# Performance work log

Measured on AMD Instinct MI355X. Metric: run time of the kernel, lower is better.

## Reference

```python
import jax, jax.numpy as jnp
import numpy as np

N = 200000      # total nodes
E = 800000      # directed edges
G = 4096        # graphs in batch
D_DRUG = 128
D_CELL = 954
HID = 128
OUT = 128
EPS = 1e-5      # BatchNorm eps


def _bn(x, gamma, beta):
    # training-mode BatchNorm1d (batch statistics, biased var), dropout is eval/identity
    m = jnp.mean(x, axis=0)
    v = jnp.mean((x - m) ** 2, axis=0)
    return gamma * (x - m) * jax.lax.rsqrt(v + EPS) + beta


def _gcn_conv(x, edge_index, W, b):
    # PyG GCNConv: add self-loops, symmetric normalization, aggregate, then bias
    src = jnp.concatenate([edge_index[0], jnp.arange(N)])
    dst = jnp.concatenate([edge_index[1], jnp.arange(N)])
    ones = jnp.ones(src.shape[0], dtype=x.dtype)
    deg = jax.ops.segment_sum(ones, dst, num_segments=N)
    dinv = jnp.where(deg > 0, jax.lax.rsqrt(jnp.maximum(deg, 1.0)), 0.0)
    norm = dinv[src] * dinv[dst]                      # [E+N]
    h = x @ W                                         # [N, out]
    msg = h[src] * norm[:, None]                      # gather + scale
    out = jax.ops.segment_sum(msg, dst, num_segments=N)  # scatter-add
    return out + b


def setup_inputs() -> dict:
    key = jax.random.key(0)
    ks = jax.random.split(key, 12)
    x = jax.random.normal(ks[0], (N, D_DRUG), jnp.float32)
    edge_index = jax.random.randint(ks[1], (2, E), 0, N)
    ibatch = (jnp.arange(N) * G) // N  # sorted, every graph non-empty
    gexpr = jax.random.normal(ks[2], (G, D_CELL), jnp.float32)

    def w(k, shape):
        return jax.random.normal(k, shape, jnp.float32) / np.float32(np.sqrt(shape[0]))

    return {
        "x": x, "edge_index": edge_index, "ibatch": ibatch, "gexpr": gexpr,
        "W1": w(ks[3], (D_DRUG, HID)), "b1": jnp.zeros((HID,), jnp.float32),
        "g1": jnp.ones((HID,), jnp.float32), "be1": jnp.zeros((HID,), jnp.float32),
        "W2": w(ks[4], (HID, OUT)), "b2": jnp.zeros((OUT,), jnp.float32),
        "g2": jnp.ones((OUT,), jnp.float32), "be2": jnp.zeros((OUT,), jnp.float32),
        "Wc1": w(ks[5], (D_CELL, HID)), "bc1": jnp.zeros((HID,), jnp.float32),
        "gc": jnp.ones((HID,), jnp.float32), "bec": jnp.zeros((HID,), jnp.float32),
        "Wc2": w(ks[6], (HID, OUT)), "bc2": jnp.zeros((OUT,), jnp.float32),
    }


def reference(x, edge_index, ibatch, gexpr,
              W1, b1, g1, be1, W2, b2, g2, be2,
              Wc1, bc1, gc, bec, Wc2, bc2):
    # drug branch
    h = _gcn_conv(x, edge_index, W1, b1)
    h = _bn(jax.nn.relu(h), g1, be1)
    h = _gcn_conv(h, edge_index, W2, b2)
    h = _bn(jax.nn.relu(h), g2, be2)
    x_drug = jax.ops.segment_max(h, ibatch, num_segments=G)  # global_max_pool
    # cellline branch
    c = jnp.tanh(gexpr @ Wc1 + bc1)
    c = _bn(c, gc, bec)
    x_cell = jax.nn.relu(c @ Wc2 + bc2)
    return x_drug, x_cell
```

## Files before the change

kernel.cpp:

```cpp
#include <hip/hip_runtime.h>

#define NFEAT 128

typedef __attribute__((ext_vector_type(4))) float f32x4;
typedef __attribute__((ext_vector_type(8))) short bf16x8;

__device__ __forceinline__ unsigned short f2bf(float f) {
    unsigned u = __builtin_bit_cast(unsigned, f);
    u += 0x7fffu + ((u >> 16) & 1u);
    return (unsigned short)(u >> 16);
}
__device__ __forceinline__ float bf2f(unsigned short s) {
    unsigned u = ((unsigned)s) << 16;
    return __builtin_bit_cast(float, u);
}

__device__ __forceinline__ void dma16(const void* g, void* l) {
    __builtin_amdgcn_global_load_lds(
        (const __attribute__((address_space(1))) unsigned int*)g,
        (__attribute__((address_space(3))) unsigned int*)l, 16, 0, 0);
}

template <int ACT, typename OutT, typename AT>
__device__ __forceinline__ void gemm_loop(
    int tfirst, int tstride, int tcount, int by,
    const AT* __restrict__ A, const unsigned short* __restrict__ Bt,
    OutT* __restrict__ C, int M, int ldA, int ldB,
    const float* __restrict__ bias, const float* __restrict__ dscale, char* smem)
{
    constexpr bool AF32 = (sizeof(AT) == 4);
    AT* buf0 = (AT*)smem;
    AT* buf1 = buf0 + 64 * 128;
    const int tid = threadIdx.x;
    const int wv = tid >> 6, lane = tid & 63;
    const int l16 = lane & 15, quad = lane >> 4;
    const int kbase = by * 128;

    const int nc0 = (wv & 1) * 64;
    bf16x8 bfr[4][4];
#pragma unroll
    for (int nt = 0; nt < 4; ++nt) {
        const unsigned short* bp =
            Bt + (size_t)(nc0 + nt * 16 + l16) * ldB + kbase + quad * 8;
#pragma unroll
        for (int ks = 0; ks < 4; ++ks)
            bfr[nt][ks] = *(const bf16x8*)(bp + ks * 32);
    }

    C += (size_t)by * M * NFEAT;
    const int rh = wv >> 1;
    const int r0 = wv * 16;

    auto stage = [&](AT* dst, long tile) {
        const long t0 = tile * 64;
        if constexpr (AF32) {
#pragma unroll
            for (int j = 0; j < 8; ++j) {
                const float* gp = (const float*)A +
                    (size_t)(t0 + r0 + j * 2 + (lane >> 5)) * ldA + kbase +
                    (lane & 31) * 4;
                dma16(gp, (void*)&dst[(r0 + j * 2) * 128]);
            }
        } else {
#pragma unroll
            for (int j = 0; j < 4; ++j) {
                const unsigned short* gp = (const unsigned short*)A +
                    (size_t)(t0 + r0 + j * 4 + (lane >> 4)) * ldA + kbase +
                    l16 * 8;
                dma16(gp, (void*)&dst[(r0 + j * 4) * 128]);
            }
        }
    };

    if (tfirst < tcount) stage(buf0, tfirst);
    __syncthreads();

    int cur = 0;
    for (long t = tfirst; t < tcount; t += tstride) {
        AT* bufc = cur ? buf1 : buf0;
        AT* bufn = cur ? buf0 : buf1;
        const long tn = t + tstride;
        if (tn < tcount) stage(bufn, tn);

        bf16x8 af[2][4];
#pragma unroll
        for (int mt = 0; mt < 2; ++mt) {
            const int row = rh * 32 + mt * 16 + l16;
#pragma unroll
            for (int ks = 0; ks < 4; ++ks) {
                if constexpr (AF32) {
                    const float* lp = (const float*)bufc + row * 128 + ks * 32 + quad * 8;
                    f32x4 v0 = *(const f32x4*)lp;
                    f32x4 v1 = *(const f32x4*)(lp + 4);
                    bf16x8 tt;
                    tt[0] = (short)f2bf(v0[0]); tt[1] = (short)f2bf(v0[1]);
                    tt[2] = (short)f2bf(v0[2]); tt[3] = (short)f2bf(v0[3]);
                    tt[4] = (short)f2bf(v1[0]); tt[5] = (short)f2bf(v1[1]);
                    tt[6] = (short)f2bf(v1[2]); tt[7] = (short)f2bf(v1[3]);
                    af[mt][ks] = tt;
                } else {
                    af[mt][ks] = *(const bf16x8*)((const unsigned short*)bufc +
                                                  row * 128 + ks * 32 + quad * 8);
                }
            }
        }

        f32x4 acc[2][4];
#pragma unroll
        for (int a = 0; a < 2; ++a)
#pragma unroll
            for (int b = 0; b < 4; ++b) acc[a][b] = (f32x4){0.f, 0.f, 0.f, 0.f};
#pragma unroll
        for (int ks = 0; ks < 4; ++ks)
#pragma unroll
            for (int nt = 0; nt < 4; ++nt)
#pragma unroll
                for (int mt = 0; mt < 2; ++mt)
                    acc[mt][nt] = __builtin_amdgcn_mfma_f32_16x16x32_bf16(
                        af[mt][ks], bfr[nt][ks], acc[mt][nt], 0, 0, 0);

        const long tile0 = t * 64;
        float ds[2][4];
#pragma unroll
        for (int mt = 0; mt < 2; ++mt)
#pragma unroll
            for (int r = 0; r < 4; ++r) {
                long row = tile0 + rh * 32 + mt * 16 + quad * 4 + r;
                ds[mt][r] = dscale ? dscale[row] : 1.f;
            }
#pragma unroll
        for (int nt = 0; nt < 4; ++nt) {
            int col = nc0 + nt * 16 + l16;
            float bv = bias ? bias[col] : 0.f;
#pragma unroll
            for (int mt = 0; mt < 2; ++mt) {
                long rbase = tile0 + rh * 32 + mt * 16 + quad * 4;
#pragma unroll
                for (int r = 0; r < 4; ++r) {
                    float v = acc[mt][nt][r] + bv;
                    if (ACT == 1) v = tanhf(v);
                    if (ACT == 2) v = fmaxf(v, 0.f);
                    v *= ds[mt][r];
                    if constexpr (sizeof(OutT) == 2)
                        C[(size_t)(rbase + r) * NFEAT + col] = (OutT)f2bf(v);
                    else
                        C[(size_t)(rbase + r) * NFEAT + col] = (OutT)v;
                }
            }
        }
        __syncthreads();
        cur ^= 1;
    }
}

__global__ void k_prep(const float* __restrict__ W1, unsigned short* __restrict__ W1t,
                       const float* __restrict__ Wc1, unsigned short* __restrict__ Wc1t,
                       const float* __restrict__ gexpr, float* __restrict__ Apad,
                       const int* __restrict__ dst, int* __restrict__ deg,
                       int G, int DC, int DCP, int E, int r1, int r2, int r3)
{
    int b = blockIdx.x, t = threadIdx.x;
    if (b < r1) {
        int idx = b * 256 + t;
        int n = idx >> 7, k = idx & 127;
        W1t[idx] = f2bf(W1[(size_t)k * NFEAT + n]);
    } else if (b < r2) {
        int idx = (b - r1) * 256 + t;
        int n = idx >> 10, k = idx & 1023;
        Wc1t[idx] = (k < DC) ? f2bf(Wc1[(size_t)k * NFEAT + n]) : (unsigned short)0;
    } else if (b < r3) {
        long idx = (long)(b - r2) * 256 + t;
        if (idx < (long)G * DCP) {
            long i = idx / DCP; int k = (int)(idx - i * DCP);
            Apad[idx] = (k < DC) ? gexpr[i * DC + k] : 0.f;
        }
    } else {
        int e = (b - r3) * 256 + t;
        if (e < E) atomicAdd(&deg[dst[e]], 1);
    }
}

__device__ __forceinline__ void bnfold_body(
    int bb, const float* __restrict__ sums8, const float* __restrict__ gamma,
    const float* __restrict__ beta, float invN,
    const float* __restrict__ W, const float* __restrict__ extra,
    unsigned short* __restrict__ Wt, float* __restrict__ brow)
{
    __shared__ float ssc[128], ssh[128];
    int t = threadIdx.x;
    if (t < 128) {
        float s = 0.f, s2 = 0.f;
#pragma unroll
        for (int c = 0; c < 8; ++c) { s += sums8[c * 256 + t]; s2 += sums8[c * 256 + 128 + t]; }
        float mean = s * invN;
        float var = s2 * invN - mean * mean;
        float rstd = rsqrtf(fmaxf(var, 0.f) + 1e-5f);
        float sc = gamma[t] * rstd;
        ssc[t] = sc;
        ssh[t] = beta[t] - mean * sc;
    }
    __syncthreads();
    if (bb < 64) {
        int idx = bb * 256 + t;
        int n = idx >> 7, k = idx & 127;
        Wt[idx] = f2bf(W[(size_t)k * NFEAT + n] * ssc[k]);
    } else if (t < 128) {
        float s = extra ? extra[t] : 0.f;
        for (int k = 0; k < 128; ++k) s += ssh[k] * W[(size_t)k * NFEAT + t];
        brow[t] = s;
    }
}

__global__ void k_bnfold2(
    const float* sA, const float* gA, const float* bA, float invA,
    const float* WA, const float* eA, unsigned short* WtA, float* browA,
    const float* sB, const float* gB, const float* bB, float invB,
    const float* WB, const float* eB, unsigned short* WtB, float* browB)
{
    int b = blockIdx.x;
    if (b < 65) bnfold_body(b, sA, gA, bA, invA, WA, eA, WtA, browA);
    else        bnfold_body(b - 65, sB, gB, bB, invB, WB, eB, WtB, browB);
}

__global__ __launch_bounds__(256) void k_scan1(const int* __restrict__ deg,
        int* __restrict__ rowptr, int* __restrict__ bsum, float* __restrict__ dinv, int N)
{
    __shared__ int sh[256];
    int t = threadIdx.x;
    int base = blockIdx.x * 1024 + t * 4;
    int v[4];
#pragma unroll
    for (int j = 0; j < 4; ++j) {
        v[j] = (base + j < N) ? deg[base + j] : 0;
        if (base + j < N) dinv[base + j] = rsqrtf((float)(v[j] + 1));
    }
    int s = v[0] + v[1] + v[2] + v[3];
    sh[t] = s;
    __syncthreads();
    int incl = s;
    for (int off = 1; off < 256; off <<= 1) {
        int x = (t >= off) ? sh[t - off] : 0;
        __syncthreads();
        incl += x;
        sh[t] = incl;
        __syncthreads();
    }
    int run = incl - s;
#pragma unroll
    for (int j = 0; j < 4; ++j) {
        if (base + j < N) rowptr[base + j] = run;
        run += v[j];
    }
    if (t == 255) bsum[blockIdx.x] = incl;
}

__global__ void k_scan2(int* __restrict__ bsum, int nb)
{
    __shared__ int sh[256];
    int t = threadIdx.x;
    int s = (t < nb) ? bsum[t] : 0;
    sh[t] = s;
    __syncthreads();
    int incl = s;
    for (int off = 1; off < 256; off <<= 1) {
        int x = (t >= off) ? sh[t - off] : 0;
        __syncthreads();
        incl += x;
        sh[t] = incl;
        __syncthreads();
    }
    if (t < nb) bsum[t] = incl - s;
}

__global__ void k_scan3(int* __restrict__ rowptr, int* __restrict__ cursor,
                        const int* __restrict__ bsum, int N, int E)
{
    int i = blockIdx.x * 256 + threadIdx.x;
    if (i < N) {
        int v = rowptr[i] + bsum[i >> 10];
        rowptr[i] = v;
        cursor[i] = v;
    } else if (i == N) {
        rowptr[N] = E;
    }
}

__global__ void k_fill(const int* __restrict__ src, const int* __restrict__ dst,
                       int* __restrict__ cursor, int* __restrict__ csr, int E)
{
    int e = blockIdx.x * 256 + threadIdx.x;
    if (e < E) {
        int pos = atomicAdd(&cursor[dst[e]], 1);
        csr[pos] = src[e];
    }
}

__global__ __launch_bounds__(256) void k_pair1(
    const float* __restrict__ x, const unsigned short* __restrict__ W1t,
    unsigned short* __restrict__ h, int N, const float* __restrict__ dinv,
    const float* __restrict__ Apad, const unsigned short* __restrict__ Wc1t,
    float* __restrict__ pbuf, int G, int nb1, int gtiles)
{
    extern __shared__ char smem[];
    int b = blockIdx.x;
    if (b < nb1) {
        gemm_loop<0, unsigned short, float>(b, nb1, gtiles, 0,
                                            x, W1t, h, N, 128, 128,
                                            nullptr, dinv, smem);
    } else {
        int cb = b - nb1;
        gemm_loop<0, float, float>(cb & 15, 16, 64, cb >> 4,
                                   Apad, Wc1t, pbuf, G, 1024, 1024,
                                   nullptr, nullptr, smem);
    }
}

__device__ __forceinline__ void unpack_add(float* acc, uint4 a)
{
    acc[0] += bf2f((unsigned short)(a.x & 0xffff));
    acc[1] += bf2f((unsigned short)(a.x >> 16));
    acc[2] += bf2f((unsigned short)(a.y & 0xffff));
    acc[3] += bf2f((unsigned short)(a.y >> 16));
    acc[4] += bf2f((unsigned short)(a.z & 0xffff));
    acc[5] += bf2f((unsigned short)(a.z >> 16));
    acc[6] += bf2f((unsigned short)(a.w & 0xffff));
    acc[7] += bf2f((unsigned short)(a.w >> 16));
}

__device__ __forceinline__ void row_gather(const unsigned short* __restrict__ h,
    const int* __restrict__ rowptr, const int* __restrict__ csr,
    long i, int f, float* acc)
{
    int lo = rowptr[i], hi = rowptr[i + 1];
    int e = lo;
    for (; e + 3 < hi; e += 4) {
        int s0 = csr[e], s1 = csr[e + 1], s2 = csr[e + 2], s3 = csr[e + 3];
        uint4 a = *(const uint4*)(h + ((size_t)s0 << 7) + f);
        uint4 b = *(const uint4*)(h + ((size_t)s1 << 7) + f);
        uint4 c = *(const uint4*)(h + ((size_t)s2 << 7) + f);
        uint4 d = *(const uint4*)(h + ((size_t)s3 << 7) + f);
        unpack_add(acc, a); unpack_add(acc, b);
        unpack_add(acc, c); unpack_add(acc, d);
    }
    for (; e < hi; ++e) {
        int s0 = csr[e];
        uint4 a = *(const uint4*)(h + ((size_t)s0 << 7) + f);
        unpack_add(acc, a);
    }
    uint4 hs = *(const uint4*)(h + ((size_t)i << 7) + f);
    unpack_add(acc, hs);
}

__global__ __launch_bounds__(256) void k_pair2(
    const unsigned short* __restrict__ h, const int* __restrict__ rowptr,
    const int* __restrict__ csr, const float* __restrict__ dinv,
    const float* __restrict__ bias, unsigned short* __restrict__ out,
    float* __restrict__ sums8, int N, int na,
    const float* __restrict__ p, const float* __restrict__ biasC,
    unsigned short* __restrict__ cbuf, float* __restrict__ sumsC, int G)
{
    __shared__ float red[4][256];
    const int tid = threadIdx.x;
    if (blockIdx.x >= na) {
        int bb = blockIdx.x - na;
        int j = tid & 127;
        int slot = bb * 2 + (tid >> 7);
        const int nslots = 64;
        const size_t st = (size_t)G * NFEAT;
        float b = biasC[j], s = 0.f, s2 = 0.f;
        for (int i = slot; i < G; i += nslots) {
            size_t o = (size_t)i * NFEAT + j;
            float v = b;
#pragma unroll
            for (int c = 0; c < 8; ++c) v += p[o + c * st];
            v = tanhf(v);
            cbuf[o] = f2bf(v);
            s += v; s2 += v * v;
        }
        atomicAdd(&sumsC[(bb & 7) * 256 + j], s);
        atomicAdd(&sumsC[(bb & 7) * 256 + 128 + j], s2);
        return;
    }
    const int wv = tid >> 6, lane = tid & 63;
    const int f = (tid & 15) << 3;
    const long g0 = (long)blockIdx.x * 16 + (tid >> 4);
    const long gstride = (long)na * 16;

    f32x4 b0 = *(const f32x4*)&bias[f];
    f32x4 b1 = *(const f32x4*)&bias[f + 4];

    float s8[8], q8[8];
#pragma unroll
    for (int j = 0; j < 8; ++j) { s8[j] = 0.f; q8[j] = 0.f; }

    for (long i = g0; i < N; i += gstride) {
        float acc[8];
#pragma unroll
        for (int j = 0; j < 8; ++j) acc[j] = 0.f;
        row_gather(h, rowptr, csr, i, f, acc);

        float di = dinv[i];
        unsigned short o[8];
#pragma unroll
        for (int j = 0; j < 8; ++j) {
            float bj = (j < 4) ? b0[j] : b1[j - 4];
            float v = fmaxf(di * acc[j] + bj, 0.f);
            o[j] = f2bf(v);
            s8[j] += v; q8[j] += v * v;
        }
        *(uint4*)(out + (i << 7) + f) = *(const uint4*)o;
    }

#pragma unroll
    for (int j = 0; j < 8; ++j) {
        s8[j] += __shfl_xor(s8[j], 16);
        s8[j] += __shfl_xor(s8[j], 32);
        q8[j] += __shfl_xor(q8[j], 16);
        q8[j] += __shfl_xor(q8[j], 32);
    }
    if (lane < 16) {
#pragma unroll
        for (int j = 0; j < 8; ++j) {
            red[wv][f + j] = s8[j];
            red[wv][128 + f + j] = q8[j];
        }
    }
    __syncthreads();
    float tot = red[0][tid] + red[1][tid] + red[2][tid] + red[3][tid];
    atomicAdd(&sums8[(blockIdx.x & 7) * 256 + tid], tot);
}

__global__ __launch_bounds__(256) void k_pair4(
    const unsigned short* __restrict__ agg, const unsigned short* __restrict__ W2t,
    unsigned short* __restrict__ h, int N, const float* __restrict__ brow2,
    const float* __restrict__ dinv,
    const unsigned short* __restrict__ cbuf, const unsigned short* __restrict__ Wc2t,
    float* __restrict__ outc, int G, const float* __restrict__ browC,
    int nb2, int gtiles)
{
    extern __shared__ char smem[];
    int b = blockIdx.x;
    if (b < nb2) {
        gemm_loop<0, unsigned short, unsigned short>(b, nb2, gtiles, 0,
                                                     agg, W2t, h, N, 128, 128,
                                                     brow2, dinv, smem);
    } else {
        gemm_loop<2, float, unsigned short>(b - nb2, 64, 64, 0,
                                            cbuf, Wc2t, outc, G, 128, 128,
                                            browC, nullptr, smem);
    }
}

__global__ __launch_bounds__(256) void k_aggmax(
    const unsigned short* __restrict__ h, const int* __restrict__ rowptr,
    const int* __restrict__ csr, const float* __restrict__ dinv,
    const float* __restrict__ bias, int* __restrict__ gmax, int* __restrict__ gmin,
    float* __restrict__ sums8, int N, int G)
{
    __shared__ float red[4][256];
    __shared__ int lmax[288], lmin[288];
    const int tid = threadIdx.x;
    const int wv = tid >> 6, lane = tid & 63;
    const int f8 = tid & 15;
    const int f = f8 << 3;
    const int grp = tid >> 4;
    const int g_lo = blockIdx.x * 2;
    const int rstart = (int)(((long long)g_lo * N + G - 1) / G);
    const int rend   = (int)(((long long)(g_lo + 2) * N + G - 1) / G);
    const int bnd1   = (int)(((long long)(g_lo + 1) * N + G - 1) / G);

    for (int idx = tid; idx < 288; idx += 256) {
        lmax[idx] = 0;
        lmin[idx] = 0x7f800000;
    }
    __syncthreads();

    f32x4 b0 = *(const f32x4*)&bias[f];
    f32x4 b1 = *(const f32x4*)&bias[f + 4];

    float s8[8], q8[8], rmx[8], rmn[8];
#pragma unroll
    for (int j = 0; j < 8; ++j) {
        s8[j] = 0.f; q8[j] = 0.f;
        rmx[j] = 0.f; rmn[j] = __builtin_bit_cast(float, 0x7f800000);
    }
    int cur = 0;

    for (long i = rstart + grp; i < rend; i += 16) {
        float acc[8];
#pragma unroll
        for (int j = 0; j < 8; ++j) acc[j] = 0.f;
        row_gather(h, rowptr, csr, i, f, acc);

        float di = dinv[i];
        int gi = (i >= bnd1);
        if (gi != cur) {
#pragma unroll
            for (int j = 0; j < 8; ++j) {
                atomicMax(&lmax[cur * 144 + j * 16 + f8], __builtin_bit_cast(int, rmx[j]));
                atomicMin(&lmin[cur * 144 + j * 16 + f8], __builtin_bit_cast(int, rmn[j]));
                rmx[j] = 0.f; rmn[j] = __builtin_bit_cast(float, 0x7f800000);
            }
            cur = gi;
        }
#pragma unroll
        for (int j = 0; j < 8; ++j) {
            float bj = (j < 4) ? b0[j] : b1[j - 4];
            float v = fmaxf(di * acc[j] + bj, 0.f);
            s8[j] += v; q8[j] += v * v;
            rmx[j] = fmaxf(rmx[j], v);
            rmn[j] = fminf(rmn[j], v);
        }
    }
#pragma unroll
    for (int j = 0; j < 8; ++j) {
        atomicMax(&lmax[cur * 144 + j * 16 + f8], __builtin_bit_cast(int, rmx[j]));
        atomicMin(&lmin[cur * 144 + j * 16 + f8], __builtin_bit_cast(int, rmn[j]));
    }

#pragma unroll
    for (int j = 0; j < 8; ++j) {
        s8[j] += __shfl_xor(s8[j], 16);
        s8[j] += __shfl_xor(s8[j], 32);
        q8[j] += __shfl_xor(q8[j], 16);
        q8[j] += __shfl_xor(q8[j], 32);
    }
    if (lane < 16) {
#pragma unroll
        for (int j = 0; j < 8; ++j) {
            red[wv][f + j] = s8[j];
            red[wv][128 + f + j] = q8[j];
        }
    }
    __syncthreads();
    float tot = red[0][tid] + red[1][tid] + red[2][tid] + red[3][tid];
    atomicAdd(&sums8[(blockIdx.x & 7) * 256 + tid], tot);

    for (int idx = tid; idx < 2 * 128; idx += 256) {
        int gg = idx >> 7, feat = idx & 127;
        int a = gg * 144 + (feat & 7) * 16 + (feat >> 3);
        gmax[(size_t)(g_lo + gg) * 128 + feat] = lmax[a];
        gmin[(size_t)(g_lo + gg) * 128 + feat] = lmin[a];
    }
}

__global__ void k_segfin(const float* __restrict__ sums8, const float* __restrict__ gamma,
                         const float* __restrict__ beta, const int* __restrict__ gmax,
                         const int* __restrict__ gmin, float* __restrict__ out,
                         float invN, int total)
{
    __shared__ float ssc[128], ssh[128];
    int t = threadIdx.x;
    if (t < 128) {
        float s = 0.f, s2 = 0.f;
#pragma unroll
        for (int c = 0; c < 8; ++c) { s += sums8[c * 256 + t]; s2 += sums8[c * 256 + 128 + t]; }
        float mean = s * invN;
        float var = s2 * invN - mean * mean;
        float rstd = rsqrtf(fmaxf(var, 0.f) + 1e-5f);
        float sc = gamma[t] * rstd;
        ssc[t] = sc;
        ssh[t] = beta[t] - mean * sc;
    }
    __syncthreads();
    int idx = blockIdx.x * 256 + t;
    if (idx < total) {
        int j = idx & 127;
        float sc = ssc[j], sh = ssh[j];
        int bits = (sc >= 0.f) ? gmax[idx] : gmin[idx];
        out[idx] = sc * __builtin_bit_cast(float, bits) + sh;
    }
}

extern "C" void kernel_launch(void* const* d_in, const int* in_sizes, int n_in,
                              void* d_out, int out_size, void* d_ws, size_t ws_size,
                              hipStream_t stream)
{
    const float* x     = (const float*)d_in[0];
    const int*   ei    = (const int*)d_in[1];
    const float* gexpr = (const float*)d_in[3];
    const float* W1  = (const float*)d_in[4];
    const float* b1  = (const float*)d_in[5];
    const float* g1  = (const float*)d_in[6];
    const float* be1 = (const float*)d_in[7];
    const float* W2  = (const float*)d_in[8];
    const float* b2  = (const float*)d_in[9];
    const float* g2  = (const float*)d_in[10];
    const float* be2 = (const float*)d_in[11];
    const float* Wc1 = (const float*)d_in[12];
    const float* bc1 = (const float*)d_in[13];
    const float* gc  = (const float*)d_in[14];
    const float* bec = (const float*)d_in[15];
    const float* Wc2 = (const float*)d_in[16];
    const float* bc2 = (const float*)d_in[17];

    const int N = in_sizes[0] / NFEAT;
    const int E = in_sizes[1] / 2;
    const int G = in_sizes[3] / 954;
    const int DC = 954, DCP = 1024;

    char* wsp = (char*)d_ws;
    size_t off = 0;
    auto alloc = [&](size_t bytes) -> char* {
        char* p = wsp + off;
        off += (bytes + 255) & ~(size_t)255;
        return p;
    };
    unsigned short* agg    = (unsigned short*)alloc((size_t)N * NFEAT * 2);
    unsigned short* h      = (unsigned short*)alloc((size_t)N * NFEAT * 2);
    float*          dinv   = (float*)alloc((size_t)N * 4);
    int*            deg    = (int*)alloc((size_t)N * 4);
    int*            rowptr = (int*)alloc((size_t)(N + 1) * 4);
    int*            cursor = (int*)alloc((size_t)N * 4);
    int*            csr    = (int*)alloc((size_t)E * 4);
    int*            bsum   = (int*)alloc(256 * 4);
    float*          Apad   = (float*)alloc((size_t)G * DCP * 4);
    float*          pbuf   = (float*)alloc((size_t)8 * G * NFEAT * 4);
    unsigned short* cbuf   = (unsigned short*)alloc((size_t)G * NFEAT * 2);
    int*            gmax   = (int*)alloc((size_t)G * NFEAT * 4);
    int*            gmin   = (int*)alloc((size_t)G * NFEAT * 4);
    unsigned short* W1t    = (unsigned short*)alloc(128 * 128 * 2);
    unsigned short* W2t    = (unsigned short*)alloc(128 * 128 * 2);
    unsigned short* Wc1t   = (unsigned short*)alloc(128 * DCP * 2);
    unsigned short* Wc2t   = (unsigned short*)alloc(128 * 128 * 2);
    float*          stats  = (float*)alloc(8192 * 4);
    float* sums1 = stats,         * sums2 = stats + 2048, * sumsC = stats + 4096;
    float* brow2  = stats + 6400, * browC  = stats + 6528;

    hipMemsetAsync(stats, 0, 6144 * 4, stream);
    hipMemsetAsync(deg, 0, (size_t)N * 4, stream);

    const int* esrc = ei;
    const int* edst = ei + E;

    const int r1 = 64;
    const int r2 = r1 + 512;
    const int r3 = r2 + (int)(((long)G * DCP + 255) / 256);
    const int rtot = r3 + (E + 255) / 256;
    k_prep<<<rtot, 256, 0, stream>>>(W1, W1t, Wc1, Wc1t, gexpr, Apad,
                                     edst, deg, G, DC, DCP, E, r1, r2, r3);

    const int nb = (N + 1023) / 1024;
    k_scan1<<<nb, 256, 0, stream>>>(deg, rowptr, bsum, dinv, N);
    k_scan2<<<1, 256, 0, stream>>>(bsum, nb);
    k_scan3<<<(N + 1 + 255) / 256, 256, 0, stream>>>(rowptr, cursor, bsum, N, E);

    k_fill<<<(E + 255) / 256, 256, 0, stream>>>(esrc, edst, cursor, csr, E);

    const int gtiles = N / 64;
    const int ablocks = 2048;
    const int NB1 = 512;
    const int NB2 = 768;

    k_pair1<<<NB1 + 128, 256, 2 * 64 * 128 * 4, stream>>>(
        x, W1t, h, N, dinv,
        Apad, Wc1t, pbuf, G, NB1, gtiles);

    k_pair2<<<ablocks + 32, 256, 0, stream>>>(
        h, rowptr, csr, dinv, b1, agg, sums1, N, ablocks,
        pbuf, bc1, cbuf, sumsC, G);

    k_bnfold2<<<130, 256, 0, stream>>>(
        sums1, g1, be1, 1.f / (float)N, W2, nullptr, W2t, brow2,
        sumsC, gc, bec, 1.f / (float)G, Wc2, bc2, Wc2t, browC);

    float* outp = (float*)d_out;
    k_pair4<<<NB2 + 64, 256, 2 * 64 * 128 * 2, stream>>>(
        agg, W2t, h, N, brow2, dinv,
        cbuf, Wc2t, outp + (size_t)G * NFEAT, G, browC, NB2, gtiles);

    k_aggmax<<<G / 2, 256, 0, stream>>>(h, rowptr, csr, dinv, b2, gmax, gmin, sums2, N, G);

    k_segfin<<<(G * NFEAT + 255) / 256, 256, 0, stream>>>(
        sums2, g2, be2, gmax, gmin, outp, 1.f / (float)N, G * NFEAT);
}
```

Measured before the change: 457.1 us.

## Pre-convert GEMM A inputs to bf16 and fuse conversion with CSR fill

Converts x to bf16 in a new kernel that interleaves conversion blocks with the CSR fill blocks, and writes the padded gexpr matrix as bf16 in the prep kernel. The first GEMM then stages bf16 tiles, which halves LDS use and removes the per-tile f32 to bf16 conversion. The block count for the x GEMM doubles. In exchange there is an extra full pass that reads x and writes a bf16 copy of it.

```diff
diff --git a/kernel.cpp b/kernel.cpp
--- a/kernel.cpp
+++ b/kernel.cpp
@@ -21,16 +21,15 @@
         (__attribute__((address_space(3))) unsigned int*)l, 16, 0, 0);
 }
 
-template <int ACT, typename OutT, typename AT>
+template <int ACT, typename OutT>
 __device__ __forceinline__ void gemm_loop(
     int tfirst, int tstride, int tcount, int by,
-    const AT* __restrict__ A, const unsigned short* __restrict__ Bt,
+    const unsigned short* __restrict__ A, const unsigned short* __restrict__ Bt,
     OutT* __restrict__ C, int M, int ldA, int ldB,
     const float* __restrict__ bias, const float* __restrict__ dscale, char* smem)
 {
-    constexpr bool AF32 = (sizeof(AT) == 4);
-    AT* buf0 = (AT*)smem;
-    AT* buf1 = buf0 + 64 * 128;
+    unsigned short* buf0 = (unsigned short*)smem;
+    unsigned short* buf1 = buf0 + 64 * 128;
     const int tid = threadIdx.x;
     const int wv = tid >> 6, lane = tid & 63;
     const int l16 = lane & 15, quad = lane >> 4;
@@ -51,24 +50,13 @@
     const int rh = wv >> 1;
     const int r0 = wv * 16;
 
-    auto stage = [&](AT* dst, long tile) {
+    auto stage = [&](unsigned short* dst, long tile) {
         const long t0 = tile * 64;
-        if constexpr (AF32) {
-#pragma unroll
-            for (int j = 0; j < 8; ++j) {
-                const float* gp = (const float*)A +
-                    (size_t)(t0 + r0 + j * 2 + (lane >> 5)) * ldA + kbase +
-                    (lane & 31) * 4;
-                dma16(gp, (void*)&dst[(r0 + j * 2) * 128]);
-            }
-        } else {
-#pragma unroll
-            for (int j = 0; j < 4; ++j) {
-                const unsigned short* gp = (const unsigned short*)A +
-                    (size_t)(t0 + r0 + j * 4 + (lane >> 4)) * ldA + kbase +
-                    l16 * 8;
-                dma16(gp, (void*)&dst[(r0 + j * 4) * 128]);
-            }
+#pragma unroll
+        for (int j = 0; j < 4; ++j) {
+            const unsigned short* gp = A +
+                (size_t)(t0 + r0 + j * 4 + (lane >> 4)) * ldA + kbase + l16 * 8;
+            dma16(gp, (void*)&dst[(r0 + j * 4) * 128]);
         }
     };
 
@@ -77,8 +65,8 @@
 
     int cur = 0;
     for (long t = tfirst; t < tcount; t += tstride) {
-        AT* bufc = cur ? buf1 : buf0;
-        AT* bufn = cur ? buf0 : buf1;
+        unsigned short* bufc = cur ? buf1 : buf0;
+        unsigned short* bufn = cur ? buf0 : buf1;
         const long tn = t + tstride;
         if (tn < tcount) stage(bufn, tn);
 
@@ -87,22 +75,8 @@
         for (int mt = 0; mt < 2; ++mt) {
             const int row = rh * 32 + mt * 16 + l16;
 #pragma unroll
-            for (int ks = 0; ks < 4; ++ks) {
-                if constexpr (AF32) {
-                    const float* lp = (const float*)bufc + row * 128 + ks * 32 + quad * 8;
-                    f32x4 v0 = *(const f32x4*)lp;
-                    f32x4 v1 = *(const f32x4*)(lp + 4);
-                    bf16x8 tt;
-                    tt[0] = (short)f2bf(v0[0]); tt[1] = (short)f2bf(v0[1]);
-                    tt[2] = (short)f2bf(v0[2]); tt[3] = (short)f2bf(v0[3]);
-                    tt[4] = (short)f2bf(v1[0]); tt[5] = (short)f2bf(v1[1]);
-                    tt[6] = (short)f2bf(v1[2]); tt[7] = (short)f2bf(v1[3]);
-                    af[mt][ks] = tt;
-                } else {
-                    af[mt][ks] = *(const bf16x8*)((const unsigned short*)bufc +
-                                                  row * 128 + ks * 32 + quad * 8);
-                }
-            }
+            for (int ks = 0; ks < 4; ++ks)
+                af[mt][ks] = *(const bf16x8*)(bufc + row * 128 + ks * 32 + quad * 8);
         }
 
         f32x4 acc[2][4];
@@ -155,7 +129,7 @@
 
 __global__ void k_prep(const float* __restrict__ W1, unsigned short* __restrict__ W1t,
                        const float* __restrict__ Wc1, unsigned short* __restrict__ Wc1t,
-                       const float* __restrict__ gexpr, float* __restrict__ Apad,
+                       const float* __restrict__ gexpr, unsigned short* __restrict__ Apadh,
                        const int* __restrict__ dst, int* __restrict__ deg,
                        int G, int DC, int DCP, int E, int r1, int r2, int r3)
 {
@@ -172,7 +146,7 @@
         long idx = (long)(b - r2) * 256 + t;
         if (idx < (long)G * DCP) {
             long i = idx / DCP; int k = (int)(idx - i * DCP);
-            Apad[idx] = (k < DC) ? gexpr[i * DC + k] : 0.f;
+            Apadh[idx] = (k < DC) ? f2bf(gexpr[i * DC + k]) : (unsigned short)0;
         }
     } else {
         int e = (b - r3) * 256 + t;
@@ -285,33 +259,58 @@
     }
 }
 
-__global__ void k_fill(const int* __restrict__ src, const int* __restrict__ dst,
-                       int* __restrict__ cursor, int* __restrict__ csr, int E)
-{
-    int e = blockIdx.x * 256 + threadIdx.x;
-    if (e < E) {
-        int pos = atomicAdd(&cursor[dst[e]], 1);
-        csr[pos] = src[e];
+__global__ void k_fillconv(const int* __restrict__ src, const int* __restrict__ dst,
+                           int* __restrict__ cursor, int* __restrict__ csr, int E, int nf,
+                           const float* __restrict__ x, unsigned short* __restrict__ xb,
+                           long nfloat)
+{
+    const int b = blockIdx.x;
+    int role, idx;
+    if (b < 2 * nf) { role = b & 1; idx = b >> 1; }
+    else            { role = 0;     idx = b - nf; }
+
+    if (role == 1) {
+        int e = idx * 256 + threadIdx.x;
+        if (e < E) {
+            int pos = atomicAdd(&cursor[dst[e]], 1);
+            csr[pos] = src[e];
+        }
+    } else {
+        long base = (long)idx * 4096 + (long)threadIdx.x * 16;
+        if (base < nfloat) {
+            f32x4 v0 = *(const f32x4*)(x + base);
+            f32x4 v1 = *(const f32x4*)(x + base + 4);
+            f32x4 v2 = *(const f32x4*)(x + base + 8);
+            f32x4 v3 = *(const f32x4*)(x + base + 12);
+            unsigned short o[16];
+#pragma unroll
+            for (int j = 0; j < 4; ++j) {
+                o[j] = f2bf(v0[j]); o[4 + j] = f2bf(v1[j]);
+                o[8 + j] = f2bf(v2[j]); o[12 + j] = f2bf(v3[j]);
+            }
+            *(uint4*)(xb + base) = *(const uint4*)&o[0];
+            *(uint4*)(xb + base + 8) = *(const uint4*)&o[8];
+        }
     }
 }
 
 __global__ __launch_bounds__(256) void k_pair1(
-    const float* __restrict__ x, const unsigned short* __restrict__ W1t,
+    const unsigned short* __restrict__ xb, const unsigned short* __restrict__ W1t,
     unsigned short* __restrict__ h, int N, const float* __restrict__ dinv,
-    const float* __restrict__ Apad, const unsigned short* __restrict__ Wc1t,
+    const unsigned short* __restrict__ Apadh, const unsigned short* __restrict__ Wc1t,
     float* __restrict__ pbuf, int G, int nb1, int gtiles)
 {
     extern __shared__ char smem[];
     int b = blockIdx.x;
     if (b < nb1) {
-        gemm_loop<0, unsigned short, float>(b, nb1, gtiles, 0,
-                                            x, W1t, h, N, 128, 128,
-                                            nullptr, dinv, smem);
+        gemm_loop<0, unsigned short>(b, nb1, gtiles, 0,
+                                     xb, W1t, h, N, 128, 128,
+                                     nullptr, dinv, smem);
     } else {
         int cb = b - nb1;
-        gemm_loop<0, float, float>(cb & 15, 16, 64, cb >> 4,
-                                   Apad, Wc1t, pbuf, G, 1024, 1024,
-                                   nullptr, nullptr, smem);
+        gemm_loop<0, float>(cb & 15, 16, 64, cb >> 4,
+                            Apadh, Wc1t, pbuf, G, 1024, 1024,
+                            nullptr, nullptr, smem);
     }
 }
 
@@ -441,13 +440,13 @@
     extern __shared__ char smem[];
     int b = blockIdx.x;
     if (b < nb2) {
-        gemm_loop<0, unsigned short, unsigned short>(b, nb2, gtiles, 0,
-                                                     agg, W2t, h, N, 128, 128,
-                                                     brow2, dinv, smem);
+        gemm_loop<0, unsigned short>(b, nb2, gtiles, 0,
+                                     agg, W2t, h, N, 128, 128,
+                                     brow2, dinv, smem);
     } else {
-        gemm_loop<2, float, unsigned short>(b - nb2, 64, 64, 0,
-                                            cbuf, Wc2t, outc, G, 128, 128,
-                                            browC, nullptr, smem);
+        gemm_loop<2, float>(b - nb2, 64, 64, 0,
+                            cbuf, Wc2t, outc, G, 128, 128,
+                            browC, nullptr, smem);
     }
 }
 
@@ -608,13 +607,14 @@
     };
     unsigned short* agg    = (unsigned short*)alloc((size_t)N * NFEAT * 2);
     unsigned short* h      = (unsigned short*)alloc((size_t)N * NFEAT * 2);
+    unsigned short* xb     = (unsigned short*)alloc((size_t)N * NFEAT * 2);
     float*          dinv   = (float*)alloc((size_t)N * 4);
     int*            deg    = (int*)alloc((size_t)N * 4);
     int*            rowptr = (int*)alloc((size_t)(N + 1) * 4);
     int*            cursor = (int*)alloc((size_t)N * 4);
     int*            csr    = (int*)alloc((size_t)E * 4);
     int*            bsum   = (int*)alloc(256 * 4);
-    float*          Apad   = (float*)alloc((size_t)G * DCP * 4);
+    unsigned short* Apadh  = (unsigned short*)alloc((size_t)G * DCP * 2);
     float*          pbuf   = (float*)alloc((size_t)8 * G * NFEAT * 4);
     unsigned short* cbuf   = (unsigned short*)alloc((size_t)G * NFEAT * 2);
     int*            gmax   = (int*)alloc((size_t)G * NFEAT * 4);
@@ -637,7 +637,7 @@
     const int r2 = r1 + 512;
     const int r3 = r2 + (int)(((long)G * DCP + 255) / 256);
     const int rtot = r3 + (E + 255) / 256;
-    k_prep<<<rtot, 256, 0, stream>>>(W1, W1t, Wc1, Wc1t, gexpr, Apad,
+    k_prep<<<rtot, 256, 0, stream>>>(W1, W1t, Wc1, Wc1t, gexpr, Apadh,
                                      edst, deg, G, DC, DCP, E, r1, r2, r3);
 
     const int nb = (N + 1023) / 1024;
@@ -645,16 +645,20 @@
     k_scan2<<<1, 256, 0, stream>>>(bsum, nb);
     k_scan3<<<(N + 1 + 255) / 256, 256, 0, stream>>>(rowptr, cursor, bsum, N, E);
 
-    k_fill<<<(E + 255) / 256, 256, 0, stream>>>(esrc, edst, cursor, csr, E);
-
     const int gtiles = N / 64;
+    const int nf = (E + 255) / 256;
+    const long nfloat = (long)N * NFEAT;
+    const int nconv = (int)((nfloat + 4095) / 4096);
     const int ablocks = 2048;
-    const int NB1 = 512;
+    const int NB1 = 1024;
     const int NB2 = 768;
 
-    k_pair1<<<NB1 + 128, 256, 2 * 64 * 128 * 4, stream>>>(
-        x, W1t, h, N, dinv,
-        Apad, Wc1t, pbuf, G, NB1, gtiles);
+    k_fillconv<<<nf + nconv, 256, 0, stream>>>(
+        esrc, edst, cursor, csr, E, nf, x, xb, nfloat);
+
+    k_pair1<<<NB1 + 128, 256, 2 * 64 * 128 * 2, stream>>>(
+        xb, W1t, h, N, dinv,
+        Apadh, Wc1t, pbuf, G, NB1, gtiles);
 
     k_pair2<<<ablocks + 32, 256, 0, stream>>>(
         h, rowptr, csr, dinv, b1, agg, sums1, N, ablocks,
```

Result: faster. 441.3 us, median of 2 (-3.4%).
